# Optimization experiments

Hardware: AMD Instinct MI355X
Metric: run time of the kernel (lower is better)

The kernel has to match this reference:

```python
import jax, jax.numpy as jnp
import numpy as np


def setup_inputs() -> dict:
    key = jax.random.key(0)
    ks = jax.random.split(key, 6)
    b, t, k, h = 8, 128, 128, 4
    q_x = jax.random.normal(ks[0], (b, t, k), dtype=jnp.float32)
    kv_x = jax.random.normal(ks[1], (b, t, t - 1, k), dtype=jnp.float32)
    s = 1.0 / np.sqrt(k).astype(np.float32)
    Wk = jax.random.normal(ks[2], (k, k), dtype=jnp.float32) * s  # tokeys.weight
    Wq = jax.random.normal(ks[3], (k, k), dtype=jnp.float32) * s  # toqueries.weight
    Wv = jax.random.normal(ks[4], ((1 + k) * h, 2 * k), dtype=jnp.float32) * (1.0 / np.sqrt(2 * k).astype(np.float32))  # tovalues.weight
    bv = jax.random.normal(ks[5], ((1 + k) * h,), dtype=jnp.float32) * 0.01  # tovalues.bias
    return dict(q_x=q_x, kv_x=kv_x, Wk=Wk, Wq=Wq, Wv=Wv, bv=bv)


def reference(q_x, kv_x, Wk, Wq, Wv, bv):
    # kv_x: (b, t, t-1, k); q_x: (b, t, k)
    b, t, m, k = kv_x.shape  # m == t - 1
    h = Wv.shape[0] // (k + 1)
    # torch Linear: y = x @ W.T
    keys = jnp.einsum('btmk,jk->btmj', kv_x, Wk)          # (b,t,m,k)
    queries = jnp.einsum('btk,jk->btj', q_x, Wq)          # (b,t,k)
    queries = jnp.broadcast_to(queries[:, :, None, :], (b, t, m, k))
    value_input = jnp.concatenate([keys, queries], axis=-1)  # (b,t,m,2k)
    vals = jnp.einsum('btmc,oc->btmo', value_input, Wv) + bv  # (b,t,m,(1+k)h)
    vals = vals.reshape(b, t, m, h, k + 1)
    score = vals[..., 0]        # (b,t,m,h)
    values = vals[..., 1:]      # (b,t,m,h,k)
    w = jax.nn.softmax(score, axis=2)  # softmax over the t-1 (pair) axis
    x = jnp.einsum('btmh,btmhk->bthk', w, values)  # weighted sum over pairs
    return x.reshape(b, t, h * k)
```

## Files before the change

kernel.cpp:

```cpp
#include <hip/hip_runtime.h>

#define KD 128
#define NH 4
#define MM 127
#define NO 516

#define OFF_W1S 0
#define OFF_WC  512
#define OFF_C   (512 + 131072)

__global__ void precompute_w(const float* __restrict__ Wk,
                             const float* __restrict__ Wq,
                             const float* __restrict__ Wv,
                             float* __restrict__ ws) {
    int o = blockIdx.x;
    int k = threadIdx.x;
    const float* wvrow = Wv + o * 256;
    float acc1 = 0.f, acc2 = 0.f;
    #pragma unroll 8
    for (int j = 0; j < 128; ++j) {
        acc1 += wvrow[j]       * Wk[j * 128 + k];
        acc2 += wvrow[128 + j] * Wq[j * 128 + k];
    }
    int h = o / 129;
    int r = o - h * 129;
    if (r == 0) {
        ws[OFF_W1S + h * 128 + k] = acc1;
    } else {
        int dd = r - 1;
        ws[OFF_WC + (size_t)(h * 256 + k) * 128 + dd]       = acc1;
        ws[OFF_WC + (size_t)(h * 256 + 128 + k) * 128 + dd] = acc2;
    }
}

__global__ __launch_bounds__(256, 2)
void attn_csum(const float* __restrict__ kv_x, float* __restrict__ ws) {
    __shared__ float skv[MM * KD];
    __shared__ float ssc[512];
    __shared__ float swt[512];
    __shared__ float cpart[2][512];

    const int bt  = blockIdx.x;
    const int tid = threadIdx.x;
    const int dq  = tid & 31;
    const int g   = tid >> 5;

    float4 w1s[NH];
    #pragma unroll
    for (int h = 0; h < NH; ++h)
        w1s[h] = *(const float4*)(ws + OFF_W1S + h * KD + dq * 4);

    const float4* src = (const float4*)(kv_x + (size_t)bt * MM * KD);
    const int bit4 = (tid >> 4) & 1;
    const int bit3 = (tid >> 3) & 1;
    const int myh  = bit4 * 2 + bit3;

    #pragma unroll
    for (int k = 0; k < 16; ++k) {
        int idx = tid + k * 256;
        int m   = g + 8 * k;
        bool valid = (m < MM);
        float4 v = valid ? src[idx] : make_float4(0.f, 0.f, 0.f, 0.f);
        if (valid) *(float4*)&skv[m * KD + dq * 4] = v;
        float p0 = v.x*w1s[0].x + v.y*w1s[0].y + v.z*w1s[0].z + v.w*w1s[0].w;
        float p1 = v.x*w1s[1].x + v.y*w1s[1].y + v.z*w1s[1].z + v.w*w1s[1].w;
        float p2 = v.x*w1s[2].x + v.y*w1s[2].y + v.z*w1s[2].z + v.w*w1s[2].w;
        float p3 = v.x*w1s[3].x + v.y*w1s[3].y + v.z*w1s[3].z + v.w*w1s[3].w;
        float x = bit4 ? p0 : p2;
        float y = bit4 ? p1 : p3;
        float a = (bit4 ? p2 : p0) + __shfl_xor(x, 16);
        float b = (bit4 ? p3 : p1) + __shfl_xor(y, 16);
        float z = bit3 ? a : b;
        float vr = (bit3 ? b : a) + __shfl_xor(z, 8);
        vr += __shfl_xor(vr, 4);
        vr += __shfl_xor(vr, 2);
        vr += __shfl_xor(vr, 1);
        if ((tid & 7) == 0 && valid) ssc[m * 4 + myh] = vr;
    }
    __syncthreads();

    {
        int h = tid >> 6, lane = tid & 63;
        float v0 = ssc[lane * 4 + h];
        bool has1 = (lane + 64) < MM;
        float v1 = has1 ? ssc[(lane + 64) * 4 + h] : -1e30f;
        float mx = fmaxf(v0, v1);
        #pragma unroll
        for (int off = 32; off; off >>= 1) mx = fmaxf(mx, __shfl_xor(mx, off));
        float e0 = __expf(v0 - mx);
        float e1 = has1 ? __expf(v1 - mx) : 0.f;
        float s = e0 + e1;
        #pragma unroll
        for (int off = 32; off; off >>= 1) s += __shfl_xor(s, off);
        float inv = 1.f / s;
        swt[lane * 4 + h] = e0 * inv;
        if (has1) swt[(lane + 64) * 4 + h] = e1 * inv;
    }
    __syncthreads();

    {
        const int ch = (tid >> 5) & 3;
        const int mh = tid >> 7;
        const int m0 = mh ? 64 : 0;
        const int m1 = mh ? MM : 64;
        float4 fa = make_float4(0.f, 0.f, 0.f, 0.f);
        #pragma unroll 8
        for (int m = m0; m < m1; ++m) {
            float w = swt[m * 4 + ch];
            float4 kq = *(const float4*)&skv[m * KD + dq * 4];
            fa.x += w * kq.x; fa.y += w * kq.y;
            fa.z += w * kq.z; fa.w += w * kq.w;
        }
        *(float4*)&cpart[mh][ch * KD + dq * 4] = fa;
    }
    __syncthreads();

    if (tid < 128) {
        float4 a = *(const float4*)&cpart[0][tid * 4];
        float4 b = *(const float4*)&cpart[1][tid * 4];
        float4 s;
        s.x = a.x + b.x; s.y = a.y + b.y; s.z = a.z + b.z; s.w = a.w + b.w;
        *(float4*)(ws + OFF_C + (size_t)bt * 512 + tid * 4) = s;
    }
}

#define BM 32
#define BN 64
#define BK 64
#define AP 34
#define BP 68

__global__ __launch_bounds__(256, 2)
void proj_out(const float* __restrict__ q_x,
              const float* __restrict__ bv,
              const float* __restrict__ ws,
              float* __restrict__ out) {
    __shared__ float sAT[BK][AP];
    __shared__ float sB[BK][BP];

    const int r0  = blockIdx.x * BM;
    const int dd0 = blockIdx.y * BN;
    const int h   = blockIdx.z;
    const int tid = threadIdx.x;
    const int tx  = tid & 15;
    const int ty  = tid >> 4;
    const float* cmat = ws + OFF_C;
    const float* Wct  = ws + OFF_WC;

    float acc[2][4];
    #pragma unroll
    for (int i = 0; i < 2; ++i)
        #pragma unroll
        for (int j = 0; j < 4; ++j) acc[i][j] = 0.f;

    for (int ks = 0; ks < 4; ++ks) {
        int kk0 = ks * BK;
        const float* Abase; int Astride;
        if (kk0 < 128) { Abase = cmat + h * KD + kk0; Astride = 512; }
        else           { Abase = q_x + (kk0 - 128);   Astride = KD;  }
        #pragma unroll
        for (int i = 0; i < 2; ++i) {
            int idx = tid + i * 256;
            int r = idx >> 4, c4 = idx & 15;
            float4 v = *(const float4*)(Abase + (size_t)(r0 + r) * Astride + c4 * 4);
            sAT[c4 * 4 + 0][r] = v.x;
            sAT[c4 * 4 + 1][r] = v.y;
            sAT[c4 * 4 + 2][r] = v.z;
            sAT[c4 * 4 + 3][r] = v.w;
        }
        #pragma unroll
        for (int i = 0; i < 4; ++i) {
            int idx = tid + i * 256;
            int c = idx >> 4, d4 = idx & 15;
            *(float4*)&sB[c][d4 * 4] =
                *(const float4*)(Wct + (size_t)(h * 256 + kk0 + c) * 128 + dd0 + d4 * 4);
        }
        __syncthreads();
        #pragma unroll 8
        for (int c = 0; c < BK; ++c) {
            float2 a  = *(const float2*)&sAT[c][ty * 2];
            float4 b4 = *(const float4*)&sB[c][tx * 4];
            acc[0][0] += a.x * b4.x; acc[0][1] += a.x * b4.y;
            acc[0][2] += a.x * b4.z; acc[0][3] += a.x * b4.w;
            acc[1][0] += a.y * b4.x; acc[1][1] += a.y * b4.y;
            acc[1][2] += a.y * b4.z; acc[1][3] += a.y * b4.w;
        }
        __syncthreads();
    }
    float bb[4];
    #pragma unroll
    for (int j = 0; j < 4; ++j) bb[j] = bv[h * 129 + 1 + dd0 + tx * 4 + j];
    #pragma unroll
    for (int i = 0; i < 2; ++i) {
        float4 v;
        v.x = acc[i][0] + bb[0];
        v.y = acc[i][1] + bb[1];
        v.z = acc[i][2] + bb[2];
        v.w = acc[i][3] + bb[3];
        *(float4*)(out + (size_t)(r0 + ty * 2 + i) * 512 + h * KD + dd0 + tx * 4) = v;
    }
}

extern "C" void kernel_launch(void* const* d_in, const int* in_sizes, int n_in,
                              void* d_out, int out_size, void* d_ws, size_t ws_size,
                              hipStream_t stream) {
    const float* q_x  = (const float*)d_in[0];
    const float* kv_x = (const float*)d_in[1];
    const float* Wk   = (const float*)d_in[2];
    const float* Wq   = (const float*)d_in[3];
    const float* Wv   = (const float*)d_in[4];
    const float* bv   = (const float*)d_in[5];
    float* out = (float*)d_out;
    float* ws  = (float*)d_ws;

    int bt = in_sizes[0] / KD;

    hipLaunchKernelGGL(precompute_w, dim3(NO), dim3(128), 0, stream, Wk, Wq, Wv, ws);
    hipLaunchKernelGGL(attn_csum, dim3(bt), dim3(256), 0, stream, kv_x, ws);
    hipLaunchKernelGGL(proj_out, dim3(bt / BM, KD / BN, NH), dim3(256), 0, stream,
                       q_x, bv, ws, out);
}
```

Measured before the change: 47.93 us.

## Drop LDS staging of kv tile; re-read from global and raise occupancy

The attention kernel no longer stages the full 127x128 kv slice in LDS (about 65KB). Scores are computed from register-prefetched global loads two rows ahead, and the weighted-sum pass re-reads kv_x from global (L2) with each thread accumulating all four heads. Launch bounds rise to 4 blocks per CU, and the partials are reduced over 8 groups. The aim is higher occupancy and more latency hiding, at the cost of a second global read of kv_x.

```diff
diff --git a/kernel.cpp b/kernel.cpp
--- a/kernel.cpp
+++ b/kernel.cpp
@@ -33,12 +33,11 @@
     }
 }
 
-__global__ __launch_bounds__(256, 2)
-void attn_csum(const float* __restrict__ kv_x, float* __restrict__ ws) {
-    __shared__ float skv[MM * KD];
+__global__ __launch_bounds__(256, 4)
+void attn_bt(const float* __restrict__ kv_x, float* __restrict__ ws) {
     __shared__ float ssc[512];
     __shared__ float swt[512];
-    __shared__ float cpart[2][512];
+    __shared__ float cpart[8][512];
 
     const int bt  = blockIdx.x;
     const int tid = threadIdx.x;
@@ -55,13 +54,15 @@
     const int bit3 = (tid >> 3) & 1;
     const int myh  = bit4 * 2 + bit3;
 
+    float4 cur = src[g * 32 + dq];
+    float4 nxt = src[(g + 8) * 32 + dq];
     #pragma unroll
     for (int k = 0; k < 16; ++k) {
-        int idx = tid + k * 256;
-        int m   = g + 8 * k;
-        bool valid = (m < MM);
-        float4 v = valid ? src[idx] : make_float4(0.f, 0.f, 0.f, 0.f);
-        if (valid) *(float4*)&skv[m * KD + dq * 4] = v;
+        int mp = g + 8 * (k + 2);
+        float4 pre = make_float4(0.f, 0.f, 0.f, 0.f);
+        if (k < 14 && mp < MM) pre = src[mp * 32 + dq];
+        int m = g + 8 * k;
+        float4 v = cur;
         float p0 = v.x*w1s[0].x + v.y*w1s[0].y + v.z*w1s[0].z + v.w*w1s[0].w;
         float p1 = v.x*w1s[1].x + v.y*w1s[1].y + v.z*w1s[1].z + v.w*w1s[1].w;
         float p2 = v.x*w1s[2].x + v.y*w1s[2].y + v.z*w1s[2].z + v.w*w1s[2].w;
@@ -75,7 +76,8 @@
         vr += __shfl_xor(vr, 4);
         vr += __shfl_xor(vr, 2);
         vr += __shfl_xor(vr, 1);
-        if ((tid & 7) == 0 && valid) ssc[m * 4 + myh] = vr;
+        if ((tid & 7) == 0 && m < MM) ssc[m * 4 + myh] = vr;
+        cur = nxt; nxt = pre;
     }
     __syncthreads();
 
@@ -94,33 +96,40 @@
         for (int off = 32; off; off >>= 1) s += __shfl_xor(s, off);
         float inv = 1.f / s;
         swt[lane * 4 + h] = e0 * inv;
-        if (has1) swt[(lane + 64) * 4 + h] = e1 * inv;
+        swt[(lane + 64) * 4 + h] = has1 ? e1 * inv : 0.f;
     }
     __syncthreads();
 
-    {
-        const int ch = (tid >> 5) & 3;
-        const int mh = tid >> 7;
-        const int m0 = mh ? 64 : 0;
-        const int m1 = mh ? MM : 64;
-        float4 fa = make_float4(0.f, 0.f, 0.f, 0.f);
-        #pragma unroll 8
-        for (int m = m0; m < m1; ++m) {
-            float w = swt[m * 4 + ch];
-            float4 kq = *(const float4*)&skv[m * KD + dq * 4];
-            fa.x += w * kq.x; fa.y += w * kq.y;
-            fa.z += w * kq.z; fa.w += w * kq.w;
-        }
-        *(float4*)&cpart[mh][ch * KD + dq * 4] = fa;
-    }
+    float4 c0 = make_float4(0.f,0.f,0.f,0.f);
+    float4 c1 = make_float4(0.f,0.f,0.f,0.f);
+    float4 c2 = make_float4(0.f,0.f,0.f,0.f);
+    float4 c3 = make_float4(0.f,0.f,0.f,0.f);
+    #pragma unroll
+    for (int k = 0; k < 16; ++k) {
+        int m = g + 8 * k;
+        if (m < MM) {
+            float4 kq = src[m * 32 + dq];
+            float4 w4 = *(const float4*)&swt[m * 4];
+            c0.x += w4.x*kq.x; c0.y += w4.x*kq.y; c0.z += w4.x*kq.z; c0.w += w4.x*kq.w;
+            c1.x += w4.y*kq.x; c1.y += w4.y*kq.y; c1.z += w4.y*kq.z; c1.w += w4.y*kq.w;
+            c2.x += w4.z*kq.x; c2.y += w4.z*kq.y; c2.z += w4.z*kq.z; c2.w += w4.z*kq.w;
+            c3.x += w4.w*kq.x; c3.y += w4.w*kq.y; c3.z += w4.w*kq.z; c3.w += w4.w*kq.w;
+        }
+    }
+    *(float4*)&cpart[g][0 * KD + dq * 4] = c0;
+    *(float4*)&cpart[g][1 * KD + dq * 4] = c1;
+    *(float4*)&cpart[g][2 * KD + dq * 4] = c2;
+    *(float4*)&cpart[g][3 * KD + dq * 4] = c3;
     __syncthreads();
 
-    if (tid < 128) {
-        float4 a = *(const float4*)&cpart[0][tid * 4];
-        float4 b = *(const float4*)&cpart[1][tid * 4];
-        float4 s;
-        s.x = a.x + b.x; s.y = a.y + b.y; s.z = a.z + b.z; s.w = a.w + b.w;
-        *(float4*)(ws + OFF_C + (size_t)bt * 512 + tid * 4) = s;
+    float* cdst = ws + OFF_C + (size_t)bt * 512;
+    #pragma unroll
+    for (int rep = 0; rep < 2; ++rep) {
+        int o = tid + rep * 256;
+        float s = 0.f;
+        #pragma unroll
+        for (int gg = 0; gg < 8; ++gg) s += cpart[gg][o];
+        cdst[o] = s;
     }
 }
 
@@ -216,7 +225,7 @@
     int bt = in_sizes[0] / KD;
 
     hipLaunchKernelGGL(precompute_w, dim3(NO), dim3(128), 0, stream, Wk, Wq, Wv, ws);
-    hipLaunchKernelGGL(attn_csum, dim3(bt), dim3(256), 0, stream, kv_x, ws);
+    hipLaunchKernelGGL(attn_bt, dim3(bt), dim3(256), 0, stream, kv_x, ws);
     hipLaunchKernelGGL(proj_out, dim3(bt / BM, KD / BN, NH), dim3(256), 0, stream,
                        q_x, bv, ws, out);
 }
```

After: 42.30 us. 1.13x faster.

## Split attention over pairs into per-warp one-pass partial softmax sums with combine kernel

Applied to the files above, without the earlier changes.

Replaces the per-(b,t) block kernel that staged kv_x in shared memory with a warp-per-16-rows kernel. Each warp computes scores, exponentiates them without max subtraction, and accumulates weighted value and normalizer partials in registers. A new combine kernel sums the 8 partials per (b,t) and normalizes. This removes the large shared-memory footprint and barriers to raise occupancy and memory parallelism. In exchange it adds an extra launch, partial-sum traffic through workspace, and a risk of overflow from skipping the softmax max.

```diff
diff --git a/kernel.cpp b/kernel.cpp
--- a/kernel.cpp
+++ b/kernel.cpp
@@ -4,10 +4,13 @@
 #define NH 4
 #define MM 127
 #define NO 516
+#define NROWS (1024 * MM)
 
 #define OFF_W1S 0
 #define OFF_WC  512
-#define OFF_C   (512 + 131072)
+#define OFF_P   (512 + 131072)
+#define OFF_Z   (OFF_P + 8192 * 512)
+#define OFF_C   (OFF_Z + 32768)
 
 __global__ void precompute_w(const float* __restrict__ Wk,
                              const float* __restrict__ Wq,
@@ -33,35 +36,36 @@
     }
 }
 
-__global__ __launch_bounds__(256, 2)
-void attn_csum(const float* __restrict__ kv_x, float* __restrict__ ws) {
-    __shared__ float skv[MM * KD];
-    __shared__ float ssc[512];
-    __shared__ float swt[512];
-    __shared__ float cpart[2][512];
-
-    const int bt  = blockIdx.x;
-    const int tid = threadIdx.x;
-    const int dq  = tid & 31;
-    const int g   = tid >> 5;
+__global__ __launch_bounds__(256, 4)
+void attn_onepass(const float* __restrict__ kv_x, float* __restrict__ ws) {
+    const int tid  = threadIdx.x;
+    const int lane = tid & 63;
+    const int dq   = lane & 31;
+    const int grp  = lane >> 5;
+    const int gw   = (blockIdx.x << 2) | (tid >> 6);
+    const int bt   = gw >> 3;
+    const int wv   = gw & 7;
 
     float4 w1s[NH];
     #pragma unroll
     for (int h = 0; h < NH; ++h)
         w1s[h] = *(const float4*)(ws + OFF_W1S + h * KD + dq * 4);
 
-    const float4* src = (const float4*)(kv_x + (size_t)bt * MM * KD);
-    const int bit4 = (tid >> 4) & 1;
-    const int bit3 = (tid >> 3) & 1;
-    const int myh  = bit4 * 2 + bit3;
-
-    #pragma unroll
-    for (int k = 0; k < 16; ++k) {
-        int idx = tid + k * 256;
-        int m   = g + 8 * k;
-        bool valid = (m < MM);
-        float4 v = valid ? src[idx] : make_float4(0.f, 0.f, 0.f, 0.f);
-        if (valid) *(float4*)&skv[m * KD + dq * 4] = v;
+    const int bit4 = (lane >> 4) & 1;
+    const int bit3 = (lane >> 3) & 1;
+
+    const float4* src = (const float4*)kv_x;
+    const size_t rowbase = (size_t)bt * MM * 32;
+
+    float4 u0 = make_float4(0.f,0.f,0.f,0.f);
+    float4 u1 = u0, u2 = u0, u3 = u0, za = u0;
+
+    #pragma unroll
+    for (int j = 0; j < 8; ++j) {
+        int m = wv * 16 + 2 * j + grp;
+        size_t idx = rowbase + (size_t)(wv * 16 + 2 * j) * 32 + lane;
+        if (idx > (size_t)NROWS * 32 - 1) idx = (size_t)NROWS * 32 - 1;
+        float4 v = src[idx];
         float p0 = v.x*w1s[0].x + v.y*w1s[0].y + v.z*w1s[0].z + v.w*w1s[0].w;
         float p1 = v.x*w1s[1].x + v.y*w1s[1].y + v.z*w1s[1].z + v.w*w1s[1].w;
         float p2 = v.x*w1s[2].x + v.y*w1s[2].y + v.z*w1s[2].z + v.w*w1s[2].w;
@@ -75,53 +79,58 @@
         vr += __shfl_xor(vr, 4);
         vr += __shfl_xor(vr, 2);
         vr += __shfl_xor(vr, 1);
-        if ((tid & 7) == 0 && valid) ssc[m * 4 + myh] = vr;
-    }
-    __syncthreads();
-
-    {
-        int h = tid >> 6, lane = tid & 63;
-        float v0 = ssc[lane * 4 + h];
-        bool has1 = (lane + 64) < MM;
-        float v1 = has1 ? ssc[(lane + 64) * 4 + h] : -1e30f;
-        float mx = fmaxf(v0, v1);
-        #pragma unroll
-        for (int off = 32; off; off >>= 1) mx = fmaxf(mx, __shfl_xor(mx, off));
-        float e0 = __expf(v0 - mx);
-        float e1 = has1 ? __expf(v1 - mx) : 0.f;
-        float s = e0 + e1;
-        #pragma unroll
-        for (int off = 32; off; off >>= 1) s += __shfl_xor(s, off);
-        float inv = 1.f / s;
-        swt[lane * 4 + h] = e0 * inv;
-        if (has1) swt[(lane + 64) * 4 + h] = e1 * inv;
-    }
-    __syncthreads();
-
-    {
-        const int ch = (tid >> 5) & 3;
-        const int mh = tid >> 7;
-        const int m0 = mh ? 64 : 0;
-        const int m1 = mh ? MM : 64;
-        float4 fa = make_float4(0.f, 0.f, 0.f, 0.f);
-        #pragma unroll 8
-        for (int m = m0; m < m1; ++m) {
-            float w = swt[m * 4 + ch];
-            float4 kq = *(const float4*)&skv[m * KD + dq * 4];
-            fa.x += w * kq.x; fa.y += w * kq.y;
-            fa.z += w * kq.z; fa.w += w * kq.w;
-        }
-        *(float4*)&cpart[mh][ch * KD + dq * 4] = fa;
-    }
-    __syncthreads();
-
-    if (tid < 128) {
-        float4 a = *(const float4*)&cpart[0][tid * 4];
-        float4 b = *(const float4*)&cpart[1][tid * 4];
-        float4 s;
-        s.x = a.x + b.x; s.y = a.y + b.y; s.z = a.z + b.z; s.w = a.w + b.w;
-        *(float4*)(ws + OFF_C + (size_t)bt * 512 + tid * 4) = s;
-    }
+        int base = (lane & 32) | (lane & 7);
+        float e0 = __expf(__shfl(vr, base));
+        float e1 = __expf(__shfl(vr, base | 8));
+        float e2 = __expf(__shfl(vr, base | 16));
+        float e3 = __expf(__shfl(vr, base | 24));
+        float vf = (m < MM) ? 1.f : 0.f;
+        e0 *= vf; e1 *= vf; e2 *= vf; e3 *= vf;
+        u0.x += e0*v.x; u0.y += e0*v.y; u0.z += e0*v.z; u0.w += e0*v.w;
+        u1.x += e1*v.x; u1.y += e1*v.y; u1.z += e1*v.z; u1.w += e1*v.w;
+        u2.x += e2*v.x; u2.y += e2*v.y; u2.z += e2*v.z; u2.w += e2*v.w;
+        u3.x += e3*v.x; u3.y += e3*v.y; u3.z += e3*v.z; u3.w += e3*v.w;
+        za.x += e0; za.y += e1; za.z += e2; za.w += e3;
+    }
+    u0.x += __shfl_xor(u0.x, 32); u0.y += __shfl_xor(u0.y, 32);
+    u0.z += __shfl_xor(u0.z, 32); u0.w += __shfl_xor(u0.w, 32);
+    u1.x += __shfl_xor(u1.x, 32); u1.y += __shfl_xor(u1.y, 32);
+    u1.z += __shfl_xor(u1.z, 32); u1.w += __shfl_xor(u1.w, 32);
+    u2.x += __shfl_xor(u2.x, 32); u2.y += __shfl_xor(u2.y, 32);
+    u2.z += __shfl_xor(u2.z, 32); u2.w += __shfl_xor(u2.w, 32);
+    u3.x += __shfl_xor(u3.x, 32); u3.y += __shfl_xor(u3.y, 32);
+    u3.z += __shfl_xor(u3.z, 32); u3.w += __shfl_xor(u3.w, 32);
+    za.x += __shfl_xor(za.x, 32); za.y += __shfl_xor(za.y, 32);
+    za.z += __shfl_xor(za.z, 32); za.w += __shfl_xor(za.w, 32);
+
+    if (lane < 32) {
+        float* P = ws + OFF_P + (size_t)gw * 512;
+        *(float4*)&P[0 * KD + dq * 4] = u0;
+        *(float4*)&P[1 * KD + dq * 4] = u1;
+        *(float4*)&P[2 * KD + dq * 4] = u2;
+        *(float4*)&P[3 * KD + dq * 4] = u3;
+    }
+    if (lane == 0)
+        *(float4*)(ws + OFF_Z + (size_t)gw * 4) = za;
+}
+
+__global__ __launch_bounds__(128, 8)
+void combine_c(float* __restrict__ ws) {
+    const int bt  = blockIdx.x;
+    const int tid = threadIdx.x;
+    const int h   = tid >> 5;
+    float4 s = make_float4(0.f,0.f,0.f,0.f);
+    float zs = 0.f;
+    #pragma unroll
+    for (int p = 0; p < 8; ++p) {
+        const float* P = ws + OFF_P + (size_t)(bt * 8 + p) * 512;
+        float4 u = *(const float4*)&P[tid * 4];
+        s.x += u.x; s.y += u.y; s.z += u.z; s.w += u.w;
+        zs += ws[OFF_Z + (size_t)(bt * 8 + p) * 4 + h];
+    }
+    float inv = 1.f / zs;
+    s.x *= inv; s.y *= inv; s.z *= inv; s.w *= inv;
+    *(float4*)(ws + OFF_C + (size_t)bt * 512 + tid * 4) = s;
 }
 
 #define BM 32
@@ -216,7 +225,8 @@
     int bt = in_sizes[0] / KD;
 
     hipLaunchKernelGGL(precompute_w, dim3(NO), dim3(128), 0, stream, Wk, Wq, Wv, ws);
-    hipLaunchKernelGGL(attn_csum, dim3(bt), dim3(256), 0, stream, kv_x, ws);
+    hipLaunchKernelGGL(attn_onepass, dim3(2048), dim3(256), 0, stream, kv_x, ws);
+    hipLaunchKernelGGL(combine_c, dim3(bt), dim3(128), 0, stream, ws);
     hipLaunchKernelGGL(proj_out, dim3(bt / BM, KD / BN, NH), dim3(256), 0, stream,
                        q_x, bv, ws, out);
 }
```

New measurement: 43.39 us. 9.5% less time.
